# Kernel optimization log

Measured on AMD Instinct MI355X. Metric: run time of the kernel, lower is better.

## Reference

```python
import jax, jax.numpy as jnp
import numpy as np

EPS = 1e-5

def _ln(x, g=None, b=None):
    m = x.mean(-1, keepdims=True)
    v = x.var(-1, keepdims=True)
    y = (x - m) / jnp.sqrt(v + EPS)
    if g is not None:
        y = y * g + b
    return y

def setup_inputs() -> dict:
    B, N, D, E, NC = 32, 256, 1024, 4096, 16
    key = jax.random.key(0)
    ks = iter(jax.random.split(key, 24))
    def rn(shape, s=0.02):
        return jax.random.normal(next(ks), shape, jnp.float32) * s
    return dict(
        h=jax.random.normal(next(ks), (B, N, D), jnp.float32),
        Wpp=rn((D, E)), bpp=jnp.zeros(E), Wsp=rn((D, E)), bsp=jnp.zeros(E),
        Wq=rn((E, E)), bq=jnp.zeros(E),
        Wk=rn((E, E)), bk=jnp.zeros(E),
        Wv=rn((E, E)), bv=jnp.zeros(E),
        g_pfs=jnp.ones(D + E), b_pfs=jnp.zeros(D + E),
        Wpfs=rn((D + E, D)), bpfs=jnp.zeros(D),
        g_sfs=jnp.ones(E), b_sfs=jnp.zeros(E),
        Wsfs=rn((E, D)), bsfs=jnp.zeros(D),
        Wpc=rn((D, NC)), bpc=jnp.zeros(NC),
        Wc0=rn((NC, 8, D)), bc0=jnp.zeros((NC, 8)),
        Wc1=rn((NC, 16, D)), bc1=jnp.zeros((NC, 16)),
        Wc2=rn((NC, 32, D)), bc2=jnp.zeros((NC, 32)),
    )

def reference(h, Wpp, bpp, Wsp, bsp, Wq, bq, Wk, bk, Wv, bv,
              g_pfs, b_pfs, Wpfs, bpfs, g_sfs, b_sfs, Wsfs, bsfs,
              Wpc, bpc, Wc0, bc0, Wc1, bc1, Wc2, bc2):
    B, N, D = h.shape
    H = 4
    E = Wpp.shape[1]
    hd = E // H
    scale = hd ** -0.5
    gelu = lambda x: jax.nn.gelu(x, approximate=False)  # torch exact GELU
    pp = gelu(h @ Wpp + bpp)                  # [B,N,E]
    sp = gelu(h @ Wsp + bsp)                  # [B,N,E]
    Q = (pp @ Wq + bq).reshape(B, N, H, hd)
    K = (sp @ Wk + bk).reshape(B, N, H, hd)
    V = (sp @ Wv + bv).reshape(B, N, H, hd)
    attn = jax.nn.softmax(jnp.einsum('bqhd,bkhd->bhqk', Q, K) * scale, axis=-1)
    intf = jnp.einsum('bhqk,bkhd->bqhd', attn, V).reshape(B, N, E)
    intf = _ln(intf)                          # F.layer_norm, no affine
    pvec = _ln((_ln(jnp.concatenate([h, intf], -1), g_pfs, b_pfs) @ Wpfs + bpfs).mean(1))  # [B,D]
    svec = _ln((_ln(sp, g_sfs, b_sfs) @ Wsfs + bsfs).mean(1))                               # [B,D]
    parent_logits = pvec @ Wpc + bpc          # [B,NC]
    y_hat = jnp.argmax(parent_logits, axis=1) # argmax(softmax) == argmax(logits)
    # routed child heads: gather per-sample weight by parent argmax, batched matvec
    child = tuple(
        jnp.einsum('bd,bnd->bn', svec, W[y_hat]) + b[y_hat]
        for W, b in ((Wc0, bc0), (Wc1, bc1), (Wc2, bc2))
    )
    return (parent_logits,) + child + (pvec, svec)
```

## Files before the change

kernel.cpp:

```cpp
#include <hip/hip_runtime.h>
#include <hip/hip_bf16.h>

typedef __bf16 bf16x8 __attribute__((ext_vector_type(8)));
typedef float f32x4 __attribute__((ext_vector_type(4)));
typedef unsigned long long u64;

#define EPSV 1e-5f

__device__ __forceinline__ float bf2f(unsigned short u){
  unsigned int x = ((unsigned int)u) << 16;
  return __builtin_bit_cast(float, x);
}
__device__ __forceinline__ unsigned short f2bf(float f){
  __bf16 b = (__bf16)f;
  return __builtin_bit_cast(unsigned short, b);
}
__device__ __forceinline__ float gelu_exact(float x){
  return 0.5f * x * (1.0f + erff(x * 0.7071067811865476f));
}
__device__ __forceinline__ void gload_lds16(const void* g, void* l){
  __builtin_amdgcn_global_load_lds((const __attribute__((address_space(1))) unsigned int*)g,
                                   (__attribute__((address_space(3))) unsigned int*)l, 16, 0, 0);
}

template<int MODE>
__global__ __launch_bounds__(512, 2)
void gemm256(const unsigned short* __restrict__ A, const unsigned short* __restrict__ B,
             const float* __restrict__ bias0, const float* __restrict__ bias1,
             void* __restrict__ C0v, void* __restrict__ C1v,
             int Kd, int lda, int ldb, int ldc)
{
  __shared__ char smem[131072];
  const int t = threadIdx.x;
  const int w = t >> 6, l = t & 63;
  const int wm = w >> 2, wn = w & 3;
  const int lr = l & 15, lg = l >> 4;
  const int nbx = gridDim.x;
  const int nwg = nbx * gridDim.y;
  int bid = blockIdx.y*nbx + blockIdx.x;
  if ((nwg & 7) == 0) bid = (bid & 7)*(nwg >> 3) + (bid >> 3);
  const int bm0 = (bid / nbx) * 256, bn0 = (bid % nbx) * 256;
  const int nk = Kd >> 6;

  const int srow = t >> 3;
  const int sslot = t & 7;

  f32x4 acc[8][4];
  #pragma unroll
  for (int i=0;i<8;++i){
    #pragma unroll
    for (int j=0;j<4;++j){ f32x4 zz = {0.f,0.f,0.f,0.f}; acc[i][j] = zz; }
  }
  bf16x8 a0[4][2], a1[4][2], b0[2][2], b1[2][2];

  auto stage = [&](int kt, int mat, int hf, int q){
    if (kt >= nk) return;
    const int r_h = q*64 + srow;
    const int s_ = sslot ^ ((r_h >> 1) & 7);
    const unsigned short* gp = (mat ? B + (size_t)(bn0 + hf*128 + r_h)*ldb
                                    : A + (size_t)(bm0 + hf*128 + r_h)*lda)
                               + (kt << 6) + s_*8;
    char* lp = smem + mat*65536 + (kt&1)*32768 + hf*16384 + q*8192 + t*16;
    gload_lds16((const void*)gp, (void*)lp);
  };
  auto rdA = [&](int d, int fm, int kk)->bf16x8{
    const int r = fm*16 + lr;
    const int s_ = (kk*4 + lg) ^ ((r >> 1) & 7);
    return *(const bf16x8*)(smem + d*32768 + wm*16384 + r*128 + s_*16);
  };
  auto rdB = [&](int d, int fn, int kk)->bf16x8{
    const int r = (wn&1)*64 + fn*16 + lr;
    const int s_ = (kk*4 + lg) ^ ((r >> 1) & 7);
    return *(const bf16x8*)(smem + 65536 + d*32768 + (wn>>1)*16384 + r*128 + s_*16);
  };

  auto ktile = [&](int kt, int d){
    #pragma unroll
    for (int fm=0; fm<4; ++fm){ a0[fm][0] = rdA(d, fm, 0); a0[fm][1] = rdA(d, fm, 1); }
    #pragma unroll
    for (int fn=0; fn<2; ++fn){ b0[fn][0] = rdB(d, fn, 0); b0[fn][1] = rdB(d, fn, 1); }
    stage(kt+1, 0, 0, 1); stage(kt+1, 0, 1, 1);
    __builtin_amdgcn_s_barrier();
    __builtin_amdgcn_s_setprio(1);
    #pragma unroll
    for (int fm=0; fm<4; ++fm)
      #pragma unroll
      for (int fn=0; fn<2; ++fn)
        #pragma unroll
        for (int kk=0; kk<2; ++kk)
          acc[fm][fn] = __builtin_amdgcn_mfma_f32_16x16x32_bf16(a0[fm][kk], b0[fn][kk], acc[fm][fn], 0,0,0);
    __builtin_amdgcn_s_setprio(0);
    #pragma unroll
    for (int fn=0; fn<2; ++fn){ b1[fn][0] = rdB(d, fn+2, 0); b1[fn][1] = rdB(d, fn+2, 1); }
    __builtin_amdgcn_s_barrier();
    __builtin_amdgcn_s_setprio(1);
    #pragma unroll
    for (int fm=0; fm<4; ++fm)
      #pragma unroll
      for (int fn=0; fn<2; ++fn)
        #pragma unroll
        for (int kk=0; kk<2; ++kk)
          acc[fm][fn+2] = __builtin_amdgcn_mfma_f32_16x16x32_bf16(a0[fm][kk], b1[fn][kk], acc[fm][fn+2], 0,0,0);
    __builtin_amdgcn_s_setprio(0);
    #pragma unroll
    for (int fm=0; fm<4; ++fm){ a1[fm][0] = rdA(d, fm+4, 0); a1[fm][1] = rdA(d, fm+4, 1); }
    stage(kt+2, 0, 0, 0); stage(kt+2, 0, 1, 0);
    stage(kt+2, 1, 0, 0); stage(kt+2, 1, 1, 0);
    __builtin_amdgcn_s_barrier();
    __builtin_amdgcn_s_setprio(1);
    #pragma unroll
    for (int fm=0; fm<4; ++fm)
      #pragma unroll
      for (int fn=0; fn<2; ++fn)
        #pragma unroll
        for (int kk=0; kk<2; ++kk)
          acc[fm+4][fn+2] = __builtin_amdgcn_mfma_f32_16x16x32_bf16(a1[fm][kk], b1[fn][kk], acc[fm+4][fn+2], 0,0,0);
    __builtin_amdgcn_s_setprio(0);
    stage(kt+2, 1, 0, 1); stage(kt+2, 1, 1, 1);
    __builtin_amdgcn_s_barrier();
    __builtin_amdgcn_s_setprio(1);
    #pragma unroll
    for (int fm=0; fm<4; ++fm)
      #pragma unroll
      for (int fn=0; fn<2; ++fn)
        #pragma unroll
        for (int kk=0; kk<2; ++kk)
          acc[fm+4][fn] = __builtin_amdgcn_mfma_f32_16x16x32_bf16(a1[fm][kk], b0[fn][kk], acc[fm+4][fn], 0,0,0);
    __builtin_amdgcn_s_setprio(0);
    if (kt + 2 < nk) { asm volatile("s_waitcnt vmcnt(6)" ::: "memory"); }
    else             { asm volatile("s_waitcnt vmcnt(0)" ::: "memory"); }
  };

  stage(0,0,0,0); stage(0,0,1,0); stage(0,0,0,1); stage(0,0,1,1);
  stage(0,1,0,0); stage(0,1,1,0); stage(0,1,0,1); stage(0,1,1,1);
  stage(1,0,0,0); stage(1,0,1,0);
  stage(1,1,0,0); stage(1,1,1,0);
  stage(1,1,0,1); stage(1,1,1,1);
  asm volatile("s_waitcnt vmcnt(6)" ::: "memory");
  __builtin_amdgcn_s_barrier();

  for (int kt = 0; kt < nk; kt += 2){ ktile(kt, 0); ktile(kt+1, 1); }

  #pragma unroll
  for (int fm=0; fm<8; ++fm){
    #pragma unroll
    for (int fn=0; fn<4; ++fn){
      const int row0 = bm0 + wm*128 + fm*16 + lg*4;
      const int col  = bn0 + wn*64 + fn*16 + lr;
      f32x4 v = acc[fm][fn];
      if constexpr (MODE == 3){
        unsigned short* C = (unsigned short*)C0v;
        const float bb = bias0[col];
        u64 pack = 0;
        #pragma unroll
        for (int j=0;j<4;++j) pack |= (u64)f2bf(v[j] + bb) << (16*j);
        *(u64*)(C + (size_t)col*256 + (size_t)(row0>>8)*1048576 + (row0&255)) = pack;
      } else if constexpr (MODE == 4){
        if (col < 4096){
          unsigned short* C = (unsigned short*)C0v;
          const float bb = bias0[col];
          #pragma unroll
          for (int j=0;j<4;++j) C[(size_t)(row0+j)*ldc + col] = f2bf(v[j] + bb);
        } else {
          const int c2 = col - 4096;
          unsigned short* C = (unsigned short*)C1v;
          const float bb = bias1[c2];
          u64 pack = 0;
          #pragma unroll
          for (int j=0;j<4;++j) pack |= (u64)f2bf(v[j] + bb) << (16*j);
          *(u64*)(C + (size_t)c2*256 + (size_t)(row0>>8)*1048576 + (row0&255)) = pack;
        }
      } else {
        const bool hi = (MODE == 0) && (col >= 4096);
        unsigned short* C = (unsigned short*)(hi ? C1v : C0v);
        const int c2 = hi ? (col - 4096) : col;
        const float bb = hi ? bias1[c2] : bias0[c2];
        #pragma unroll
        for (int j=0;j<4;++j){
          float x = v[j] + bb;
          if constexpr (MODE==0) x = gelu_exact(x);
          C[(size_t)(row0+j)*ldc + c2] = f2bf(x);
        }
      }
    }
  }
}

template<int MODE>
__global__ __launch_bounds__(256)
void gemm_bt(const unsigned short* __restrict__ A, const unsigned short* __restrict__ B,
             const float* __restrict__ bias, void* __restrict__ Cv,
             int Kd, int lda, int ldb, int ldc,
             long sA2, long sA1, long sB2, long sB1, long sC2, long sC1,
             float scale)
{
  __shared__ unsigned short lds[2][2][4096];
  const int t = threadIdx.x;
  const int w = t >> 6, l = t & 63;
  const int z = blockIdx.z;
  A += (size_t)(z>>2)*sA2 + (size_t)(z&3)*sA1;
  B += (size_t)(z>>2)*sB2 + (size_t)(z&3)*sB1;
  const int bm0 = blockIdx.y * 128, bn0 = blockIdx.x * 128;
  const int nk = Kd >> 5;

  const int sr = l >> 2;
  const int ss = l & 3;

  f32x4 acc[4][4];
  #pragma unroll
  for (int i=0;i<4;++i){
    #pragma unroll
    for (int j=0;j<4;++j){ f32x4 zz = {0.f,0.f,0.f,0.f}; acc[i][j] = zz; }
  }

  const int wm = w >> 1, wn = w & 1;
  const int lr = l & 15, lg = l >> 4;

  auto stage = [&](int kt, int bb){
    const int k0 = kt << 5;
    #pragma unroll
    for (int i=0;i<2;++i){
      const int r  = w*32 + i*16 + sr;
      const int sa = ss ^ ((r>>1)&3);
      const unsigned short* ga = A + (size_t)(bm0 + r)*lda + (k0 + sa*8);
      gload_lds16((const void*)ga, (void*)((char*)&lds[bb][0][0] + w*2048 + i*1024));
      const unsigned short* gb = B + (size_t)(bn0 + r)*ldb + (k0 + sa*8);
      gload_lds16((const void*)gb, (void*)((char*)&lds[bb][1][0] + w*2048 + i*1024));
    }
  };

  int buf = 0;
  stage(0, 0);
  for (int kt=0; kt<nk; ++kt){
    __syncthreads();
    if (kt+1 < nk) stage(kt+1, buf^1);
    bf16x8 av[4], bv[4];
    #pragma unroll
    for (int fm=0; fm<4; ++fm){
      const int row = wm*64 + fm*16 + lr;
      const int sl  = lg ^ ((row>>1)&3);
      av[fm] = *(const bf16x8*)((const char*)&lds[buf][0][0] + row*64 + sl*16);
    }
    #pragma unroll
    for (int fn=0; fn<4; ++fn){
      const int col = wn*64 + fn*16 + lr;
      const int sl  = lg ^ ((col>>1)&3);
      bv[fn] = *(const bf16x8*)((const char*)&lds[buf][1][0] + col*64 + sl*16);
    }
    #pragma unroll
    for (int fm=0; fm<4; ++fm){
      #pragma unroll
      for (int fn=0; fn<4; ++fn)
        acc[fm][fn] = __builtin_amdgcn_mfma_f32_16x16x32_bf16(av[fm], bv[fn], acc[fm][fn], 0,0,0);
    }
    buf ^= 1;
  }

  const size_t coff = (size_t)(z>>2)*sC2 + (size_t)(z&3)*sC1;
  #pragma unroll
  for (int fm=0; fm<4; ++fm){
    #pragma unroll
    for (int fn=0; fn<4; ++fn){
      const int row0 = bm0 + wm*64 + fm*16 + lg*4;
      const int col  = bn0 + wn*64 + fn*16 + lr;
      f32x4 v = acc[fm][fn];
      if constexpr (MODE == 2){
        float* C = (float*)Cv + coff;
        #pragma unroll
        for (int j=0;j<4;++j) C[(size_t)(row0+j)*ldc + col] = v[j]*scale;
      }
    }
  }
}

__global__ __launch_bounds__(256)
void k_convh(const float* __restrict__ in, unsigned short* __restrict__ out){
  const size_t id = (size_t)blockIdx.x*256 + threadIdx.x;
  float4 v = ((const float4*)in)[id];
  u64 pack = (u64)f2bf(v.x) | ((u64)f2bf(v.y)<<16) | ((u64)f2bf(v.z)<<32) | ((u64)f2bf(v.w)<<48);
  *(u64*)(out + id*4) = pack;
}

__global__ __launch_bounds__(256)
void k_tconv(const float* __restrict__ W, unsigned short* __restrict__ Wt, int Kd, int N){
  __shared__ float lt[64][65];
  const int t = threadIdx.x;
  const int n0 = blockIdx.x*64, k0 = blockIdx.y*64;
  #pragma unroll
  for (int i=0;i<16;++i){
    int lin = i*256 + t; int r = lin>>6, c = lin&63;
    lt[r][c] = W[(size_t)(k0+r)*N + n0 + c];
  }
  __syncthreads();
  #pragma unroll
  for (int i=0;i<16;++i){
    int lin = i*256 + t; int n = lin>>6, k = lin&63;
    Wt[(size_t)(n0+n)*Kd + k0 + k] = f2bf(lt[k][n]);
  }
}

__global__ __launch_bounds__(256)
void k_softmax(const float* __restrict__ S, unsigned short* __restrict__ P){
  const int t = threadIdx.x, w = t>>6, l = t&63;
  const size_t row = (size_t)blockIdx.x*4 + w;
  float4 v = *(const float4*)(S + row*256 + l*4);
  float m = fmaxf(fmaxf(v.x,v.y), fmaxf(v.z,v.w));
  #pragma unroll
  for (int off=32; off; off>>=1) m = fmaxf(m, __shfl_xor(m, off));
  float e0 = expf(v.x-m), e1 = expf(v.y-m), e2 = expf(v.z-m), e3 = expf(v.w-m);
  float s = e0+e1+e2+e3;
  #pragma unroll
  for (int off=32; off; off>>=1) s += __shfl_xor(s, off);
  const float inv = 1.0f/s;
  u64 pack = (u64)f2bf(e0*inv) | ((u64)f2bf(e1*inv)<<16) | ((u64)f2bf(e2*inv)<<32) | ((u64)f2bf(e3*inv)<<48);
  *(u64*)(P + row*256 + l*4) = pack;
}

__device__ __forceinline__ void blkred2(float& a, float& b, float* sred, int t){
  #pragma unroll
  for (int off=32; off; off>>=1){ a += __shfl_xor(a, off); b += __shfl_xor(b, off); }
  __syncthreads();
  if ((t&63)==0){ sred[(t>>6)*2] = a; sred[(t>>6)*2+1] = b; }
  __syncthreads();
  a = sred[0]+sred[2]+sred[4]+sred[6];
  b = sred[1]+sred[3]+sred[5]+sred[7];
}

__global__ __launch_bounds__(256)
void k_stats(const float* __restrict__ h, const float* __restrict__ intf,
             const unsigned short* __restrict__ sp,
             const float* __restrict__ g_pfs, const float* __restrict__ b_pfs,
             const float* __restrict__ g_sfs, const float* __restrict__ b_sfs,
             float* __restrict__ part_p, float* __restrict__ part_s, int g0)
{
  __shared__ float sred[8];
  const int bl = blockIdx.x, grp = blockIdx.y, t = threadIdx.x;
  float zacc[20], wacc[16];
  #pragma unroll
  for (int j=0;j<20;++j) zacc[j]=0.f;
  #pragma unroll
  for (int j=0;j<16;++j) wacc[j]=0.f;
  for (int rr=0; rr<16; ++rr){
    const size_t r = (size_t)bl*256 + grp*16 + rr;
    float hv[4], iv[16], sv[16];
    #pragma unroll
    for (int j=0;j<4;++j) hv[j] = h[r*1024 + j*256 + t];
    float s1=0.f, s2=0.f;
    #pragma unroll
    for (int j=0;j<16;++j){ float x = intf[r*4096 + j*256 + t]; iv[j]=x; s1+=x; s2+=x*x; }
    blkred2(s1,s2,sred,t);
    const float m1 = s1*(1.f/4096.f);
    const float rs1 = rsqrtf(fmaxf(s2*(1.f/4096.f) - m1*m1, 0.f) + EPSV);
    float t1=0.f, t2=0.f;
    #pragma unroll
    for (int j=0;j<4;++j){ t1 += hv[j]; t2 += hv[j]*hv[j]; }
    #pragma unroll
    for (int j=0;j<16;++j){ float y = (iv[j]-m1)*rs1; iv[j]=y; t1+=y; t2+=y*y; }
    blkred2(t1,t2,sred,t);
    const float m2 = t1*(1.f/5120.f);
    const float rs2 = rsqrtf(fmaxf(t2*(1.f/5120.f) - m2*m2, 0.f) + EPSV);
    #pragma unroll
    for (int j=0;j<4;++j){ int idx = j*256+t; zacc[j] += ((hv[j]-m2)*rs2)*g_pfs[idx] + b_pfs[idx]; }
    #pragma unroll
    for (int j=0;j<16;++j){ int idx = 1024 + j*256+t; zacc[4+j] += ((iv[j]-m2)*rs2)*g_pfs[idx] + b_pfs[idx]; }
    float u1=0.f, u2=0.f;
    #pragma unroll
    for (int j=0;j<16;++j){ float x = bf2f(sp[r*4096 + j*256 + t]); sv[j]=x; u1+=x; u2+=x*x; }
    blkred2(u1,u2,sred,t);
    const float m3 = u1*(1.f/4096.f);
    const float rs3 = rsqrtf(fmaxf(u2*(1.f/4096.f) - m3*m3, 0.f) + EPSV);
    #pragma unroll
    for (int j=0;j<16;++j){ int idx = j*256+t; wacc[j] += ((sv[j]-m3)*rs3)*g_sfs[idx] + b_sfs[idx]; }
  }
  const size_t pb = (size_t)(g0 + bl)*16 + grp;
  #pragma unroll
  for (int j=0;j<20;++j) part_p[pb*5120 + j*256 + t] = zacc[j];
  #pragma unroll
  for (int j=0;j<16;++j) part_s[pb*4096 + j*256 + t] = wacc[j];
}

__global__ __launch_bounds__(256)
void k_reduce(const float* __restrict__ part_p, const float* __restrict__ part_s,
              float* __restrict__ xbar, float* __restrict__ ybar){
  int id = blockIdx.x*256 + threadIdx.x;
  if (id < 32*5120){
    const int b = id / 5120, i = id % 5120;
    float s = 0.f;
    for (int g=0; g<16; ++g) s += part_p[((size_t)b*16+g)*5120 + i];
    xbar[(size_t)b*5120 + i] = s * (1.f/256.f);
  } else {
    id -= 32*5120;
    const int b = id / 4096, i = id % 4096;
    float s = 0.f;
    for (int g=0; g<16; ++g) s += part_s[((size_t)b*16+g)*4096 + i];
    ybar[(size_t)b*4096 + i] = s * (1.f/256.f);
  }
}

__global__ __launch_bounds__(256)
void k_proj_part(const float* __restrict__ xbar, const float* __restrict__ ybar,
                 const float* __restrict__ Wpfs, const float* __restrict__ Wsfs,
                 float* __restrict__ pbuf){
  const int path = blockIdx.z;
  const int y = blockIdx.y;
  if (path == 1 && y >= 8) return;
  const int Kp = path ? 4096 : 5120;
  const float* X = path ? ybar : xbar;
  const float* W = path ? Wsfs : Wpfs;
  const int t = threadIdx.x;
  const int col = blockIdx.x*64 + (t & 63);
  const int sub = t >> 6;
  const int k0 = y*512 + sub*128;
  float acc[32];
  #pragma unroll
  for (int b=0;b<32;++b) acc[b] = 0.f;
  for (int i4=0; i4<32; ++i4){
    const int k = k0 + i4*4;
    float wv0 = W[(size_t)(k  )*1024 + col];
    float wv1 = W[(size_t)(k+1)*1024 + col];
    float wv2 = W[(size_t)(k+2)*1024 + col];
    float wv3 = W[(size_t)(k+3)*1024 + col];
    #pragma unroll
    for (int b=0;b<32;++b){
      float4 xv = *(const float4*)(X + (size_t)b*Kp + k);
      acc[b] += xv.x*wv0 + xv.y*wv1 + xv.z*wv2 + xv.w*wv3;
    }
  }
  float* dst = pbuf + ((size_t)(path*40 + y*4 + sub)*32)*1024 + col;
  #pragma unroll
  for (int b=0;b<32;++b) dst[(size_t)b*1024] = acc[b];
}

__global__ __launch_bounds__(256)
void k_projred(const float* __restrict__ pbuf,
               const float* __restrict__ bpfs, const float* __restrict__ bsfs,
               float* __restrict__ tpre, float* __restrict__ spre){
  const int id = blockIdx.x*256 + threadIdx.x;
  const int path = id >> 15;
  const int rem = id & 32767;
  const int b = rem >> 10, col = rem & 1023;
  const int ns = path ? 32 : 40;
  const float* src = pbuf + ((size_t)(path*40)*32 + b)*1024 + col;
  float s = path ? bsfs[col] : bpfs[col];
  for (int g=0; g<ns; ++g) s += src[(size_t)g*32*1024];
  (path ? spre : tpre)[(size_t)b*1024 + col] = s;
}

__global__ __launch_bounds__(256)
void k_lnrow(const float* __restrict__ tpre, const float* __restrict__ spre,
             float* __restrict__ out){
  __shared__ float sred[8];
  const int id = blockIdx.x, t = threadIdx.x;
  const int path = id >> 5, b = id & 31;
  const float* src = (path ? spre : tpre) + (size_t)b*1024;
  float v[4]; float s1=0.f, s2=0.f;
  #pragma unroll
  for (int j=0;j<4;++j){ v[j] = src[j*256+t]; s1 += v[j]; s2 += v[j]*v[j]; }
  blkred2(s1,s2,sred,t);
  const float m = s1*(1.f/1024.f);
  const float rs = rsqrtf(fmaxf(s2*(1.f/1024.f)-m*m,0.f)+EPSV);
  float* dst = out + (path ? 35072 : 2304) + (size_t)b*1024;
  #pragma unroll
  for (int j=0;j<4;++j) dst[j*256+t] = (v[j]-m)*rs;
}

__global__ __launch_bounds__(256)
void k_head(const float* __restrict__ Wpc, const float* __restrict__ bpc,
            const float* __restrict__ Wc0, const float* __restrict__ bc0,
            const float* __restrict__ Wc1, const float* __restrict__ bc1,
            const float* __restrict__ Wc2, const float* __restrict__ bc2,
            float* __restrict__ out){
  __shared__ float slog[16];
  __shared__ int sy;
  const int b = blockIdx.x, t = threadIdx.x, w = t>>6, l = t&63;
  const float* pv = out + 2304 + (size_t)b*1024;
  const float* sv = out + 35072 + (size_t)b*1024;
  #pragma unroll
  for (int jj=0; jj<4; ++jj){
    const int j = w*4 + jj;
    float a = 0.f;
    for (int i=l; i<1024; i+=64) a += pv[i]*Wpc[(size_t)i*16 + j];
    #pragma unroll
    for (int off=32; off; off>>=1) a += __shfl_xor(a, off);
    if (l==0){ const float lgv = a + bpc[j]; slog[j] = lgv; out[b*16 + j] = lgv; }
  }
  __syncthreads();
  if (t==0){
    int best=0; float bvv = slog[0];
    for (int i=1;i<16;++i) if (slog[i] > bvv){ bvv = slog[i]; best = i; }
    sy = best;
  }
  __syncthreads();
  const int y = sy;
  const float* Ws[3] = {Wc0, Wc1, Wc2};
  const float* bs[3] = {bc0, bc1, bc2};
  const int nouts[3] = {8,16,32};
  const int ooff[3]  = {512, 768, 1280};
  for (int hI=0; hI<3; ++hI){
    const int no = nouts[hI];
    for (int n = w; n < no; n += 4){
      const float* wr = Ws[hI] + ((size_t)y*no + n)*1024;
      float a = 0.f;
      for (int i=l; i<1024; i+=64) a += sv[i]*wr[i];
      #pragma unroll
      for (int off=32; off; off>>=1) a += __shfl_xor(a, off);
      if (l==0) out[ooff[hI] + b*no + n] = a + bs[hI][(size_t)y*no + n];
    }
  }
}

extern "C" void kernel_launch(void* const* d_in, const int* in_sizes, int n_in,
                              void* d_out, int out_size, void* d_ws, size_t ws_size,
                              hipStream_t stream)
{
  const float* h    = (const float*)d_in[0];
  const float* Wpp  = (const float*)d_in[1];
  const float* bpp  = (const float*)d_in[2];
  const float* Wsp  = (const float*)d_in[3];
  const float* bsp  = (const float*)d_in[4];
  const float* Wq   = (const float*)d_in[5];
  const float* bq   = (const float*)d_in[6];
  const float* Wk   = (const float*)d_in[7];
  const float* bk   = (const float*)d_in[8];
  const float* Wv   = (const float*)d_in[9];
  const float* bv   = (const float*)d_in[10];
  const float* g_pfs= (const float*)d_in[11];
  const float* b_pfs= (const float*)d_in[12];
  const float* Wpfs = (const float*)d_in[13];
  const float* bpfs = (const float*)d_in[14];
  const float* g_sfs= (const float*)d_in[15];
  const float* b_sfs= (const float*)d_in[16];
  const float* Wsfs = (const float*)d_in[17];
  const float* bsfs = (const float*)d_in[18];
  const float* Wpc  = (const float*)d_in[19];
  const float* bpc  = (const float*)d_in[20];
  const float* Wc0  = (const float*)d_in[21];
  const float* bc0  = (const float*)d_in[22];
  const float* Wc1  = (const float*)d_in[23];
  const float* bc1  = (const float*)d_in[24];
  const float* Wc2  = (const float*)d_in[25];
  const float* bc2  = (const float*)d_in[26];
  float* out = (float*)d_out;
  char* ws = (char*)d_ws;
  (void)in_sizes; (void)n_in; (void)out_size;

  struct PlanT { int G, NS; };
  const PlanT plans[6] = {{16,4096},{8,4096},{4,4096},{2,4096},{1,4096},{1,1024}};
  int G = 0, NS = 0;
  size_t oWt=0,oPp=0,oPs=0,oXb=0,oYb=0,oTp=0,oSp=0,oPbf=0,oHb=0,oPb=0,oSb=0,oQ=0,oK=0,oVt=0;
  for (int pi = 0; pi < 6; ++pi){
    const size_t g = plans[pi].G, ns = plans[pi].NS;
    size_t off = 0;
    auto alloc = [&](size_t bytes){ size_t o = off; off += (bytes + 255) & ~255ULL; return o; };
    size_t wt = alloc(ns*4096*2);
    size_t pp_ = alloc(32ULL*16*5120*4);
    size_t ps_ = alloc(32ULL*16*4096*4);
    size_t xb = alloc(32*5120*4);
    size_t yb = alloc(32*4096*4);
    size_t tp = alloc(32*1024*4);
    size_t sp_ = alloc(32*1024*4);
    size_t pbf = alloc(2*40*32*1024*4);
    size_t hb = alloc(g*524288);
    size_t pb = alloc(g*2097152);
    size_t sb = alloc(g*2097152);
    size_t q  = alloc(g*2097152);
    size_t k  = alloc(g*2097152);
    size_t vt = alloc(g*2097152);
    if (off <= ws_size){
      G = (int)g; NS = (int)ns;
      oWt=wt; oPp=pp_; oPs=ps_; oXb=xb; oYb=yb; oTp=tp; oSp=sp_; oPbf=pbf;
      oHb=hb; oPb=pb; oSb=sb; oQ=q; oK=k; oVt=vt;
      break;
    }
  }
  if (!G) return;

  unsigned short* Wt   = (unsigned short*)(ws + oWt);
  float* part_p = (float*)(ws + oPp);
  float* part_s = (float*)(ws + oPs);
  float* xbar   = (float*)(ws + oXb);
  float* ybar   = (float*)(ws + oYb);
  float* tpre   = (float*)(ws + oTp);
  float* spre   = (float*)(ws + oSp);
  float* pbuf   = (float*)(ws + oPbf);
  unsigned short* h_bf = (unsigned short*)(ws + oHb);
  unsigned short* pp   = (unsigned short*)(ws + oPb);
  unsigned short* sp   = (unsigned short*)(ws + oSb);
  unsigned short* Q    = (unsigned short*)(ws + oQ);
  unsigned short* Kb   = (unsigned short*)(ws + oK);
  unsigned short* Vt   = (unsigned short*)(ws + oVt);
  float*          S    = (float*)(ws + oPb);
  unsigned short* P    = (unsigned short*)(ws + oPb + (size_t)G*1048576);
  float*          intf = (float*)(ws + oQ);

  const float scale = 1.0f/32.0f;
  (void)oK;

  for (int g0 = 0; g0 < 32; g0 += G){
    const float* h_g = h + (size_t)g0*262144;

    hipLaunchKernelGGL(k_convh, dim3(G*256), dim3(256), 0, stream, h_g, h_bf);

    hipLaunchKernelGGL(k_tconv, dim3(64,16), dim3(256), 0, stream, Wpp, Wt, 1024, 4096);
    hipLaunchKernelGGL(gemm256<0>, dim3(16,G), dim3(512), 0, stream,
                       h_bf, Wt, bpp, bpp, (void*)pp, (void*)pp, 1024, 1024,1024,4096);
    for (int nso = 0; nso < 4096; nso += NS){
      hipLaunchKernelGGL(k_tconv, dim3(NS/64,64), dim3(256), 0, stream, Wq + nso, Wt, 4096, 4096);
      hipLaunchKernelGGL(gemm256<1>, dim3(NS/256,G), dim3(512), 0, stream,
                         pp, Wt, bq + nso, bq + nso, (void*)(Q + nso), (void*)(Q + nso), 4096, 4096,4096,4096);
    }
    hipLaunchKernelGGL(k_tconv, dim3(64,16), dim3(256), 0, stream, Wsp, Wt, 1024, 4096);
    hipLaunchKernelGGL(gemm256<0>, dim3(16,G), dim3(512), 0, stream,
                       h_bf, Wt, bsp, bsp, (void*)sp, (void*)sp, 1024, 1024,1024,4096);
    for (int nso = 0; nso < 4096; nso += NS){
      hipLaunchKernelGGL(k_tconv, dim3(NS/64,64), dim3(256), 0, stream, Wk + nso, Wt, 4096, 4096);
      hipLaunchKernelGGL(gemm256<1>, dim3(NS/256,G), dim3(512), 0, stream,
                         sp, Wt, bk + nso, bk + nso, (void*)(Kb + nso), (void*)(Kb + nso), 4096, 4096,4096,4096);
    }
    for (int nso = 0; nso < 4096; nso += NS){
      hipLaunchKernelGGL(k_tconv, dim3(NS/64,64), dim3(256), 0, stream, Wv + nso, Wt, 4096, 4096);
      hipLaunchKernelGGL(gemm256<3>, dim3(NS/256,G), dim3(512), 0, stream,
                         sp, Wt, bv + nso, bv + nso, (void*)(Vt + (size_t)nso*256), (void*)(Vt + (size_t)nso*256), 4096, 4096,4096,256);
    }
    hipLaunchKernelGGL(gemm_bt<2>, dim3(2,2,G*4), dim3(256), 0, stream,
                       Q, Kb, (const float*)nullptr, (void*)S, 1024, 4096,4096,256,
                       1048576L,1024L, 1048576L,1024L, 262144L,65536L, scale);
    hipLaunchKernelGGL(k_softmax, dim3(G*256), dim3(256), 0, stream, S, P);
    hipLaunchKernelGGL(gemm_bt<2>, dim3(8,2,G*4), dim3(256), 0, stream,
                       P, Vt, (const float*)nullptr, (void*)intf, 256, 256,256,4096,
                       262144L,65536L, 1048576L,262144L, 1048576L,1024L, 1.f);
    hipLaunchKernelGGL(k_stats, dim3(G,16), dim3(256), 0, stream,
                       h_g, intf, sp, g_pfs, b_pfs, g_sfs, b_sfs, part_p, part_s, g0);
  }

  hipLaunchKernelGGL(k_reduce, dim3(1152), dim3(256), 0, stream, part_p, part_s, xbar, ybar);
  hipLaunchKernelGGL(k_proj_part, dim3(16,10,2), dim3(256), 0, stream,
                     xbar, ybar, Wpfs, Wsfs, pbuf);
  hipLaunchKernelGGL(k_projred, dim3(256), dim3(256), 0, stream,
                     pbuf, bpfs, bsfs, tpre, spre);
  hipLaunchKernelGGL(k_lnrow, dim3(64), dim3(256), 0, stream, tpre, spre, out);
  hipLaunchKernelGGL(k_head, dim3(32), dim3(256), 0, stream,
                     Wpc, bpc, Wc0, bc0, Wc1, bc1, Wc2, bc2, out);
}
```

Before: 1.400 ms.

## Hoist weight transposes out of batch-group loop and reorder GEMM stage issue

Adds a workspace plan that transposes and converts all projection weights (Wpp, Wsp, Wq, Wk, Wv) to bf16 once before the batch-group loop, instead of redoing it per group. Buffers are aliased (pbuf, h_bf, pp reuse q/vt/k) to fit the larger persistent weight storage. The GEMM inner tile also issues its global-to-LDS stage loads before the LDS fragment reads, so the global loads start earlier. This costs extra workspace and adds aliasing that must not overlap live data.

```diff
diff --git a/kernel.cpp b/kernel.cpp
--- a/kernel.cpp
+++ b/kernel.cpp
@@ -75,11 +75,11 @@
   };
 
   auto ktile = [&](int kt, int d){
+    stage(kt+1, 0, 0, 1); stage(kt+1, 0, 1, 1);
     #pragma unroll
     for (int fm=0; fm<4; ++fm){ a0[fm][0] = rdA(d, fm, 0); a0[fm][1] = rdA(d, fm, 1); }
     #pragma unroll
     for (int fn=0; fn<2; ++fn){ b0[fn][0] = rdB(d, fn, 0); b0[fn][1] = rdB(d, fn, 1); }
-    stage(kt+1, 0, 0, 1); stage(kt+1, 0, 1, 1);
     __builtin_amdgcn_s_barrier();
     __builtin_amdgcn_s_setprio(1);
     #pragma unroll
@@ -102,10 +102,10 @@
         for (int kk=0; kk<2; ++kk)
           acc[fm][fn+2] = __builtin_amdgcn_mfma_f32_16x16x32_bf16(a0[fm][kk], b1[fn][kk], acc[fm][fn+2], 0,0,0);
     __builtin_amdgcn_s_setprio(0);
-    #pragma unroll
-    for (int fm=0; fm<4; ++fm){ a1[fm][0] = rdA(d, fm+4, 0); a1[fm][1] = rdA(d, fm+4, 1); }
     stage(kt+2, 0, 0, 0); stage(kt+2, 0, 1, 0);
     stage(kt+2, 1, 0, 0); stage(kt+2, 1, 1, 0);
+    #pragma unroll
+    for (int fm=0; fm<4; ++fm){ a1[fm][0] = rdA(d, fm+4, 0); a1[fm][1] = rdA(d, fm+4, 1); }
     __builtin_amdgcn_s_barrier();
     __builtin_amdgcn_s_setprio(1);
     #pragma unroll
@@ -544,31 +544,52 @@
   char* ws = (char*)d_ws;
   (void)in_sizes; (void)n_in; (void)out_size;
 
-  struct PlanT { int G, NS; };
-  const PlanT plans[6] = {{16,4096},{8,4096},{4,4096},{2,4096},{1,4096},{1,1024}};
-  int G = 0, NS = 0;
-  size_t oWt=0,oPp=0,oPs=0,oXb=0,oYb=0,oTp=0,oSp=0,oPbf=0,oHb=0,oPb=0,oSb=0,oQ=0,oK=0,oVt=0;
-  for (int pi = 0; pi < 6; ++pi){
+  struct PlanT { int G, NS, hoist; };
+  const PlanT plans[7] = {{16,4096,1},{16,4096,0},{8,4096,0},{4,4096,0},{2,4096,0},{1,4096,0},{1,1024,0}};
+  int G = 0, NS = 0, HOIST = 0;
+  size_t oWt=0,oWps=0,oWq=0,oWk2=0,oWv2=0,oSP=0;
+  size_t oPp=0,oPs=0,oXb=0,oYb=0,oTp=0,oSp=0,oPbf=0,oHb=0,oPb=0,oSb=0,oQ=0,oK=0,oVt=0;
+  for (int pi = 0; pi < 7; ++pi){
     const size_t g = plans[pi].G, ns = plans[pi].NS;
+    const int hoist = plans[pi].hoist;
     size_t off = 0;
     auto alloc = [&](size_t bytes){ size_t o = off; off += (bytes + 255) & ~255ULL; return o; };
-    size_t wt = alloc(ns*4096*2);
-    size_t pp_ = alloc(32ULL*16*5120*4);
-    size_t ps_ = alloc(32ULL*16*4096*4);
-    size_t xb = alloc(32*5120*4);
-    size_t yb = alloc(32*4096*4);
-    size_t tp = alloc(32*1024*4);
-    size_t sp_ = alloc(32*1024*4);
-    size_t pbf = alloc(2*40*32*1024*4);
-    size_t hb = alloc(g*524288);
-    size_t pb = alloc(g*2097152);
-    size_t sb = alloc(g*2097152);
-    size_t q  = alloc(g*2097152);
-    size_t k  = alloc(g*2097152);
-    size_t vt = alloc(g*2097152);
+    size_t wt=0, wps=0, wq=0, wk2=0, wv2=0, sp2=0, pbf=0, hb=0, pb=0;
+    size_t pp_, ps_, xb, yb, tp, sp_, sb, q, k, vt;
+    if (hoist){
+      wps = alloc(8192ULL*1024*2);
+      wq  = alloc(4096ULL*4096*2);
+      wk2 = alloc(4096ULL*4096*2);
+      wv2 = alloc(4096ULL*4096*2);
+      pp_ = alloc(32ULL*16*5120*4);
+      ps_ = alloc(32ULL*16*4096*4);
+      xb = alloc(32*5120*4); yb = alloc(32*4096*4);
+      tp = alloc(32*1024*4); sp_ = alloc(32*1024*4);
+      sb = alloc(g*2097152);
+      q  = alloc(g*2097152);
+      k  = alloc(g*2097152);
+      vt = alloc(g*2097152);
+      sp2 = alloc(g*1572864);
+      pbf = q; hb = vt; pb = k;
+    } else {
+      wt = alloc(ns*4096*2);
+      pp_ = alloc(32ULL*16*5120*4);
+      ps_ = alloc(32ULL*16*4096*4);
+      xb = alloc(32*5120*4); yb = alloc(32*4096*4);
+      tp = alloc(32*1024*4); sp_ = alloc(32*1024*4);
+      pbf = alloc(2*40*32*1024*4);
+      hb = alloc(g*524288);
+      pb = alloc(g*2097152);
+      sb = alloc(g*2097152);
+      q  = alloc(g*2097152);
+      k  = alloc(g*2097152);
+      vt = alloc(g*2097152);
+      sp2 = pb;
+    }
     if (off <= ws_size){
-      G = (int)g; NS = (int)ns;
-      oWt=wt; oPp=pp_; oPs=ps_; oXb=xb; oYb=yb; oTp=tp; oSp=sp_; oPbf=pbf;
+      G = (int)g; NS = (int)ns; HOIST = hoist;
+      oWt=wt; oWps=wps; oWq=wq; oWk2=wk2; oWv2=wv2; oSP=sp2;
+      oPp=pp_; oPs=ps_; oXb=xb; oYb=yb; oTp=tp; oSp=sp_; oPbf=pbf;
       oHb=hb; oPb=pb; oSb=sb; oQ=q; oK=k; oVt=vt;
       break;
     }
@@ -576,6 +597,10 @@
   if (!G) return;
 
   unsigned short* Wt   = (unsigned short*)(ws + oWt);
+  unsigned short* WpsT = (unsigned short*)(ws + oWps);
+  unsigned short* WqT  = (unsigned short*)(ws + oWq);
+  unsigned short* WkT  = (unsigned short*)(ws + oWk2);
+  unsigned short* WvT  = (unsigned short*)(ws + oWv2);
   float* part_p = (float*)(ws + oPp);
   float* part_s = (float*)(ws + oPs);
   float* xbar   = (float*)(ws + oXb);
@@ -589,38 +614,59 @@
   unsigned short* Q    = (unsigned short*)(ws + oQ);
   unsigned short* Kb   = (unsigned short*)(ws + oK);
   unsigned short* Vt   = (unsigned short*)(ws + oVt);
-  float*          S    = (float*)(ws + oPb);
-  unsigned short* P    = (unsigned short*)(ws + oPb + (size_t)G*1048576);
+  float*          S    = (float*)(ws + oSP);
+  unsigned short* P    = (unsigned short*)(ws + oSP + (size_t)G*1048576);
   float*          intf = (float*)(ws + oQ);
 
   const float scale = 1.0f/32.0f;
   (void)oK;
 
+  if (HOIST){
+    hipLaunchKernelGGL(k_tconv, dim3(64,16), dim3(256), 0, stream, Wpp, WpsT, 1024, 4096);
+    hipLaunchKernelGGL(k_tconv, dim3(64,16), dim3(256), 0, stream, Wsp, WpsT + 4096ULL*1024, 1024, 4096);
+    hipLaunchKernelGGL(k_tconv, dim3(64,64), dim3(256), 0, stream, Wq, WqT, 4096, 4096);
+    hipLaunchKernelGGL(k_tconv, dim3(64,64), dim3(256), 0, stream, Wk, WkT, 4096, 4096);
+    hipLaunchKernelGGL(k_tconv, dim3(64,64), dim3(256), 0, stream, Wv, WvT, 4096, 4096);
+  }
+
   for (int g0 = 0; g0 < 32; g0 += G){
     const float* h_g = h + (size_t)g0*262144;
 
     hipLaunchKernelGGL(k_convh, dim3(G*256), dim3(256), 0, stream, h_g, h_bf);
 
-    hipLaunchKernelGGL(k_tconv, dim3(64,16), dim3(256), 0, stream, Wpp, Wt, 1024, 4096);
-    hipLaunchKernelGGL(gemm256<0>, dim3(16,G), dim3(512), 0, stream,
-                       h_bf, Wt, bpp, bpp, (void*)pp, (void*)pp, 1024, 1024,1024,4096);
-    for (int nso = 0; nso < 4096; nso += NS){
-      hipLaunchKernelGGL(k_tconv, dim3(NS/64,64), dim3(256), 0, stream, Wq + nso, Wt, 4096, 4096);
-      hipLaunchKernelGGL(gemm256<1>, dim3(NS/256,G), dim3(512), 0, stream,
-                         pp, Wt, bq + nso, bq + nso, (void*)(Q + nso), (void*)(Q + nso), 4096, 4096,4096,4096);
-    }
-    hipLaunchKernelGGL(k_tconv, dim3(64,16), dim3(256), 0, stream, Wsp, Wt, 1024, 4096);
-    hipLaunchKernelGGL(gemm256<0>, dim3(16,G), dim3(512), 0, stream,
-                       h_bf, Wt, bsp, bsp, (void*)sp, (void*)sp, 1024, 1024,1024,4096);
-    for (int nso = 0; nso < 4096; nso += NS){
-      hipLaunchKernelGGL(k_tconv, dim3(NS/64,64), dim3(256), 0, stream, Wk + nso, Wt, 4096, 4096);
-      hipLaunchKernelGGL(gemm256<1>, dim3(NS/256,G), dim3(512), 0, stream,
-                         sp, Wt, bk + nso, bk + nso, (void*)(Kb + nso), (void*)(Kb + nso), 4096, 4096,4096,4096);
-    }
-    for (int nso = 0; nso < 4096; nso += NS){
-      hipLaunchKernelGGL(k_tconv, dim3(NS/64,64), dim3(256), 0, stream, Wv + nso, Wt, 4096, 4096);
-      hipLaunchKernelGGL(gemm256<3>, dim3(NS/256,G), dim3(512), 0, stream,
-                         sp, Wt, bv + nso, bv + nso, (void*)(Vt + (size_t)nso*256), (void*)(Vt + (size_t)nso*256), 4096, 4096,4096,256);
+    if (HOIST){
+      hipLaunchKernelGGL(gemm256<0>, dim3(16,G), dim3(512), 0, stream,
+                         h_bf, WpsT, bpp, bpp, (void*)pp, (void*)pp, 1024, 1024,1024,4096);
+      hipLaunchKernelGGL(gemm256<1>, dim3(16,G), dim3(512), 0, stream,
+                         pp, WqT, bq, bq, (void*)Q, (void*)Q, 4096, 4096,4096,4096);
+      hipLaunchKernelGGL(gemm256<0>, dim3(16,G), dim3(512), 0, stream,
+                         h_bf, WpsT + 4096ULL*1024, bsp, bsp, (void*)sp, (void*)sp, 1024, 1024,1024,4096);
+      hipLaunchKernelGGL(gemm256<1>, dim3(16,G), dim3(512), 0, stream,
+                         sp, WkT, bk, bk, (void*)Kb, (void*)Kb, 4096, 4096,4096,4096);
+      hipLaunchKernelGGL(gemm256<3>, dim3(16,G), dim3(512), 0, stream,
+                         sp, WvT, bv, bv, (void*)Vt, (void*)Vt, 4096, 4096,4096,256);
+    } else {
+      hipLaunchKernelGGL(k_tconv, dim3(64,16), dim3(256), 0, stream, Wpp, Wt, 1024, 4096);
+      hipLaunchKernelGGL(gemm256<0>, dim3(16,G), dim3(512), 0, stream,
+                         h_bf, Wt, bpp, bpp, (void*)pp, (void*)pp, 1024, 1024,1024,4096);
+      for (int nso = 0; nso < 4096; nso += NS){
+        hipLaunchKernelGGL(k_tconv, dim3(NS/64,64), dim3(256), 0, stream, Wq + nso, Wt, 4096, 4096);
+        hipLaunchKernelGGL(gemm256<1>, dim3(NS/256,G), dim3(512), 0, stream,
+                           pp, Wt, bq + nso, bq + nso, (void*)(Q + nso), (void*)(Q + nso), 4096, 4096,4096,4096);
+      }
+      hipLaunchKernelGGL(k_tconv, dim3(64,16), dim3(256), 0, stream, Wsp, Wt, 1024, 4096);
+      hipLaunchKernelGGL(gemm256<0>, dim3(16,G), dim3(512), 0, stream,
+                         h_bf, Wt, bsp, bsp, (void*)sp, (void*)sp, 1024, 1024,1024,4096);
+      for (int nso = 0; nso < 4096; nso += NS){
+        hipLaunchKernelGGL(k_tconv, dim3(NS/64,64), dim3(256), 0, stream, Wk + nso, Wt, 4096, 4096);
+        hipLaunchKernelGGL(gemm256<1>, dim3(NS/256,G), dim3(512), 0, stream,
+                           sp, Wt, bk + nso, bk + nso, (void*)(Kb + nso), (void*)(Kb + nso), 4096, 4096,4096,4096);
+      }
+      for (int nso = 0; nso < 4096; nso += NS){
+        hipLaunchKernelGGL(k_tconv, dim3(NS/64,64), dim3(256), 0, stream, Wv + nso, Wt, 4096, 4096);
+        hipLaunchKernelGGL(gemm256<3>, dim3(NS/256,G), dim3(512), 0, stream,
+                           sp, Wt, bv + nso, bv + nso, (void*)(Vt + (size_t)nso*256), (void*)(Vt + (size_t)nso*256), 4096, 4096,4096,256);
+      }
     }
     hipLaunchKernelGGL(gemm_bt<2>, dim3(2,2,G*4), dim3(256), 0, stream,
                        Q, Kb, (const float*)nullptr, (void*)S, 1024, 4096,4096,256,
```

Result: faster. 1.318 ms (-5.8%).
